# Optimization experiments

Hardware: AMD Instinct MI355X
Metric: run time of the kernel (lower is better)

## Reference

```python
import jax, jax.numpy as jnp
import numpy as np

N_EDGES = 1_000_000
N_PARTICLES = 50_000
NUM_RADIAL = 16
EMBED = 128
OUT_EMBED = 256
NUM_TARGETS = 1


def setup_inputs() -> dict:
    key = jax.random.key(0)
    ks = jax.random.split(key, 12)
    s = lambda fan_in: 1.0 / np.sqrt(fan_in)
    inp = {
        'messages': jax.random.normal(ks[0], (N_EDGES, EMBED), jnp.float32),
        'rbf': jax.random.normal(ks[1], (N_EDGES, NUM_RADIAL), jnp.float32),
        'idx_i': jax.random.randint(ks[2], (N_EDGES,), 0, N_PARTICLES),
        'idx_j': jax.random.randint(ks[3], (N_EDGES,), 0, N_PARTICLES),
        'W_rbf': jax.random.normal(ks[4], (NUM_RADIAL, EMBED), jnp.float32) * s(NUM_RADIAL),
        'W_up': jax.random.normal(ks[5], (EMBED, OUT_EMBED), jnp.float32) * s(EMBED),
        'W1': jax.random.normal(ks[6], (OUT_EMBED, OUT_EMBED), jnp.float32) * s(OUT_EMBED),
        'b1': jnp.zeros((OUT_EMBED,), jnp.float32),
        'W2': jax.random.normal(ks[7], (OUT_EMBED, OUT_EMBED), jnp.float32) * s(OUT_EMBED),
        'b2': jnp.zeros((OUT_EMBED,), jnp.float32),
        'W3': jax.random.normal(ks[8], (OUT_EMBED, OUT_EMBED), jnp.float32) * s(OUT_EMBED),
        'b3': jnp.zeros((OUT_EMBED,), jnp.float32),
        'W_final': jax.random.normal(ks[9], (OUT_EMBED, NUM_TARGETS), jnp.float32) * s(OUT_EMBED),
    }
    return inp


def reference(messages, rbf, idx_i, idx_j, W_rbf, W_up, W1, b1, W2, b2, W3, b3, W_final):
    # RBF gate: [E, NUM_RADIAL] @ [NUM_RADIAL, EMBED] -> [E, EMBED]
    transformed_rbf = rbf @ W_rbf
    gated = messages * transformed_rbf  # elementwise, [E, EMBED]
    # scatter-add per receiving atom idx_i -> [N_PARTICLES, EMBED]
    summed = jax.ops.segment_sum(gated, idx_i, num_segments=N_PARTICLES)
    h = summed @ W_up
    h = jax.nn.swish(h @ W1 + b1)
    h = jax.nn.swish(h @ W2 + b2)
    h = jax.nn.swish(h @ W3 + b3)
    per_atom_targets = h @ W_final  # [N_PARTICLES, NUM_TARGETS]
    return per_atom_targets
```

## Files before the change

kernel.cpp:

```cpp
#include <hip/hip_runtime.h>
#include <hip/hip_bf16.h>

#define EMBED 128
#define NRAD  16
#define OUTE  256

typedef __bf16 bf16x8 __attribute__((ext_vector_type(8)));
typedef float  f32x4  __attribute__((ext_vector_type(4)));

static __device__ __forceinline__ unsigned short f2bf(float x) {
    return __builtin_bit_cast(unsigned short, (__bf16)x);
}

__global__ __launch_bounds__(256) void zero_fill_kernel(uint4* __restrict__ dst, int n4)
{
    const uint4 z = {0u, 0u, 0u, 0u};
    for (int i = blockIdx.x * blockDim.x + threadIdx.x; i < n4;
         i += gridDim.x * blockDim.x)
        dst[i] = z;
}

__global__ __launch_bounds__(256) void hist_kernel(const int* __restrict__ idx_i,
                                                   int* __restrict__ counts, int n_edges)
{
    for (int e = blockIdx.x * blockDim.x + threadIdx.x; e < n_edges;
         e += gridDim.x * blockDim.x)
        atomicAdd(&counts[idx_i[e]], 1);
}

__global__ __launch_bounds__(1024) void scan_kernel(const int* __restrict__ counts,
                                                    int* __restrict__ cursor, int n)
{
    __shared__ int partial[1024];
    const int tid = threadIdx.x;
    const int chunk = (n + 1023) / 1024;
    const int lo = min(tid * chunk, n), hi = min(lo + chunk, n);
    int s = 0;
    for (int i = lo; i < hi; ++i) s += counts[i];
    partial[tid] = s;
    __syncthreads();
    for (int off = 1; off < 1024; off <<= 1) {
        int v = (tid >= off) ? partial[tid - off] : 0;
        __syncthreads();
        partial[tid] += v;
        __syncthreads();
    }
    int run = (tid > 0) ? partial[tid - 1] : 0;
    for (int i = lo; i < hi; ++i) {
        cursor[i] = run;
        run += counts[i];
    }
}

__global__ __launch_bounds__(256) void scatter_ids_kernel(const int* __restrict__ idx_i,
                                                          int* __restrict__ cursor,
                                                          int* __restrict__ edge_order,
                                                          int* __restrict__ pid_sorted,
                                                          int n_edges)
{
    for (int e = blockIdx.x * blockDim.x + threadIdx.x; e < n_edges;
         e += gridDim.x * blockDim.x) {
        const int i = idx_i[e];
        const int pos = atomicAdd(&cursor[i], 1);
        edge_order[pos] = e;
        pid_sorted[pos] = i;
    }
}

__device__ __forceinline__ float2 rbf_dot(float4 q0, float4 q1, float4 q2, float4 q3,
                                          const float2* w)
{
    const float rv[NRAD] = {q0.x, q0.y, q0.z, q0.w, q1.x, q1.y, q1.z, q1.w,
                            q2.x, q2.y, q2.z, q2.w, q3.x, q3.y, q3.z, q3.w};
    float tx = 0.f, ty = 0.f;
#pragma unroll
    for (int r = 0; r < NRAD; ++r) {
        tx = fmaf(rv[r], w[r].x, tx);
        ty = fmaf(rv[r], w[r].y, ty);
    }
    return make_float2(tx, ty);
}

#define SEGSTEP(P, M, T)                                                    \
    do {                                                                    \
        if ((P) != cur) {                                                   \
            if (first) {                                                    \
                atomicAdd(&summed[(long long)cur * EMBED + col], ax);       \
                atomicAdd(&summed[(long long)cur * EMBED + col + 1], ay);   \
                first = false;                                              \
            } else {                                                        \
                *reinterpret_cast<float2*>(                                 \
                    &summed[(long long)cur * EMBED + col]) =                \
                    make_float2(ax, ay);                                    \
            }                                                               \
            ax = 0.f; ay = 0.f; cur = (P);                                  \
        }                                                                   \
        ax = fmaf((M).x, (T).x, ax);                                        \
        ay = fmaf((M).y, (T).y, ay);                                        \
    } while (0)

__global__ __launch_bounds__(256, 4) void gated_segsum_kernel(
    const float* __restrict__ messages, const float* __restrict__ rbf,
    const int* __restrict__ edge_order, const int* __restrict__ pid_sorted,
    const float* __restrict__ W_rbf, float* __restrict__ summed, int n_edges)
{
    const int lane = threadIdx.x & 63;
    const int wv   = threadIdx.x >> 6;
    const int col  = lane * 2;

    float2 w[NRAD];
#pragma unroll
    for (int r = 0; r < NRAD; ++r)
        w[r] = *reinterpret_cast<const float2*>(&W_rbf[r * EMBED + col]);

    const int nwin = (n_edges + 63) >> 6;
    for (int win = blockIdx.x * 4 + wv; win < nwin; win += gridDim.x * 4) {
        const int w0 = win << 6;
        const int nq = min(n_edges - w0, 64);

        float ax = 0.f, ay = 0.f;
        int  cur   = pid_sorted[w0];
        bool first = true;

        int q = 0;
        for (; q + 4 <= nq; q += 4) {
            const int b = w0 + q;
            const int e0 = edge_order[b + 0];
            const int e1 = edge_order[b + 1];
            const int e2 = edge_order[b + 2];
            const int e3 = edge_order[b + 3];
            const int p0 = pid_sorted[b + 0];
            const int p1 = pid_sorted[b + 1];
            const int p2 = pid_sorted[b + 2];
            const int p3 = pid_sorted[b + 3];

            const float2 m0 = *reinterpret_cast<const float2*>(
                messages + (long long)e0 * EMBED + col);
            const float2 m1 = *reinterpret_cast<const float2*>(
                messages + (long long)e1 * EMBED + col);
            const float2 m2 = *reinterpret_cast<const float2*>(
                messages + (long long)e2 * EMBED + col);
            const float2 m3 = *reinterpret_cast<const float2*>(
                messages + (long long)e3 * EMBED + col);

            const float4* R0 = reinterpret_cast<const float4*>(rbf + (long long)e0 * NRAD);
            const float4* R1 = reinterpret_cast<const float4*>(rbf + (long long)e1 * NRAD);
            const float4* R2 = reinterpret_cast<const float4*>(rbf + (long long)e2 * NRAD);
            const float4* R3 = reinterpret_cast<const float4*>(rbf + (long long)e3 * NRAD);
            const float2 t0 = rbf_dot(R0[0], R0[1], R0[2], R0[3], w);
            const float2 t1 = rbf_dot(R1[0], R1[1], R1[2], R1[3], w);
            const float2 t2 = rbf_dot(R2[0], R2[1], R2[2], R2[3], w);
            const float2 t3 = rbf_dot(R3[0], R3[1], R3[2], R3[3], w);

            SEGSTEP(p0, m0, t0);
            SEGSTEP(p1, m1, t1);
            SEGSTEP(p2, m2, t2);
            SEGSTEP(p3, m3, t3);
        }
        for (; q < nq; ++q) {
            const int b = w0 + q;
            const int e = edge_order[b];
            const int p = pid_sorted[b];
            const float2 m = *reinterpret_cast<const float2*>(
                messages + (long long)e * EMBED + col);
            const float4* R = reinterpret_cast<const float4*>(rbf + (long long)e * NRAD);
            const float2 t = rbf_dot(R[0], R[1], R[2], R[3], w);
            SEGSTEP(p, m, t);
        }

        atomicAdd(&summed[(long long)cur * EMBED + col], ax);
        atomicAdd(&summed[(long long)cur * EMBED + col + 1], ay);
    }
}

__global__ __launch_bounds__(256) void prep_weights_kernel(
    const float* __restrict__ Wup, const float* __restrict__ W1,
    const float* __restrict__ W2, const float* __restrict__ W3,
    __bf16* __restrict__ WupT, __bf16* __restrict__ W1T,
    __bf16* __restrict__ W2T, __bf16* __restrict__ W3T)
{
    const int total = OUTE * EMBED + 3 * OUTE * OUTE;
    for (int id = blockIdx.x * blockDim.x + threadIdx.x; id < total;
         id += gridDim.x * blockDim.x) {
        if (id < OUTE * EMBED) {
            const int n = id / EMBED, k = id % EMBED;
            WupT[id] = (__bf16)Wup[k * OUTE + n];
        } else {
            const int r = id - OUTE * EMBED;
            const int wsel = r / (OUTE * OUTE);
            const int rr = r % (OUTE * OUTE);
            const int n = rr / OUTE, k = rr % OUTE;
            const float* src = (wsel == 0) ? W1 : ((wsel == 1) ? W2 : W3);
            __bf16* dst = (wsel == 0) ? W1T : ((wsel == 1) ? W2T : W3T);
            dst[rr] = (__bf16)src[k * OUTE + n];
        }
    }
}

template <int K, bool ACT>
__device__ __forceinline__ void mlp_layer(const unsigned short* lin, unsigned short* lout,
                                          const __bf16* __restrict__ Wt,
                                          const float* __restrict__ bias, int l, int w)
{
    f32x4 acc[4][4];
#pragma unroll
    for (int i = 0; i < 4; ++i)
#pragma unroll
        for (int j = 0; j < 4; ++j)
            acc[i][j] = (f32x4){0.f, 0.f, 0.f, 0.f};

    const int lr = l & 15;
    const int hi = l >> 4;
    const int kg = hi * 8;

#pragma unroll
    for (int kk = 0; kk < K; kk += 32) {
        bf16x8 af[4], bf_[4];
#pragma unroll
        for (int i = 0; i < 4; ++i) {
            const int row = i * 16 + lr;
            const int byte = row * 512 + (((kk + kg) * 2) ^ ((row & 7) << 4));
            af[i] = *reinterpret_cast<const bf16x8*>(
                reinterpret_cast<const char*>(lin) + byte);
        }
#pragma unroll
        for (int j = 0; j < 4; ++j) {
            const int n = w * 64 + j * 16 + lr;
            bf_[j] = *reinterpret_cast<const bf16x8*>(Wt + (size_t)n * K + kk + kg);
        }
#pragma unroll
        for (int i = 0; i < 4; ++i)
#pragma unroll
            for (int j = 0; j < 4; ++j)
                acc[i][j] = __builtin_amdgcn_mfma_f32_16x16x32_bf16(af[i], bf_[j],
                                                                    acc[i][j], 0, 0, 0);
    }

    float bb[4];
#pragma unroll
    for (int j = 0; j < 4; ++j)
        bb[j] = ACT ? bias[w * 64 + j * 16 + lr] : 0.f;

#pragma unroll
    for (int j = 0; j < 4; ++j) {
        const int colb = (w * 64 + j * 16 + lr) * 2;
#pragma unroll
        for (int i = 0; i < 4; ++i) {
#pragma unroll
            for (int r = 0; r < 4; ++r) {
                const int row = i * 16 + hi * 4 + r;
                float v = acc[i][j][r];
                if (ACT) {
                    v += bb[j];
                    v = v / (1.f + __expf(-v));
                }
                const int byte = row * 512 + (colb ^ ((row & 7) << 4));
                *reinterpret_cast<unsigned short*>(
                    reinterpret_cast<char*>(lout) + byte) = f2bf(v);
            }
        }
    }
}

__global__ __launch_bounds__(256) void fused_mlp_kernel(
    const float* __restrict__ summed,
    const __bf16* __restrict__ WupT, const __bf16* __restrict__ W1T,
    const __bf16* __restrict__ W2T, const __bf16* __restrict__ W3T,
    const float* __restrict__ b1, const float* __restrict__ b2,
    const float* __restrict__ b3, const float* __restrict__ Wf,
    float* __restrict__ out, int M)
{
    __shared__ __align__(16) unsigned short buf0[64 * 256];
    __shared__ __align__(16) unsigned short buf1[64 * 256];

    const int tid = threadIdx.x;
    const int l = tid & 63, w = tid >> 6;
    const int row0 = blockIdx.x * 64;

#pragma unroll
    for (int i = 0; i < 8; ++i) {
        const int id = tid + i * 256;
        const int row = id >> 5;
        const int c = (id & 31) * 4;
        float4 v = make_float4(0.f, 0.f, 0.f, 0.f);
        const int gr = row0 + row;
        if (gr < M)
            v = *reinterpret_cast<const float4*>(summed + (long long)gr * EMBED + c);
        ushort4 u = make_ushort4(f2bf(v.x), f2bf(v.y), f2bf(v.z), f2bf(v.w));
        const int byte = row * 512 + ((c * 2) ^ ((row & 7) << 4));
        *reinterpret_cast<ushort4*>(reinterpret_cast<char*>(buf0) + byte) = u;
    }
    __syncthreads();

    mlp_layer<EMBED, false>(buf0, buf1, WupT, nullptr, l, w);
    __syncthreads();
    mlp_layer<OUTE, true>(buf1, buf0, W1T, b1, l, w);
    __syncthreads();
    mlp_layer<OUTE, true>(buf0, buf1, W2T, b2, l, w);
    __syncthreads();
    mlp_layer<OUTE, true>(buf1, buf0, W3T, b3, l, w);
    __syncthreads();

    const int row = tid >> 2, q = tid & 3;
    float s = 0.f;
#pragma unroll
    for (int c = 0; c < 8; ++c) {
        const int k = q * 64 + c * 8;
        const int byte = row * 512 + ((k * 2) ^ ((row & 7) << 4));
        const bf16x8 hv = *reinterpret_cast<const bf16x8*>(
            reinterpret_cast<const char*>(buf0) + byte);
        const float4 wa = *reinterpret_cast<const float4*>(Wf + k);
        const float4 wb = *reinterpret_cast<const float4*>(Wf + k + 4);
        s += (float)hv[0] * wa.x + (float)hv[1] * wa.y +
             (float)hv[2] * wa.z + (float)hv[3] * wa.w +
             (float)hv[4] * wb.x + (float)hv[5] * wb.y +
             (float)hv[6] * wb.z + (float)hv[7] * wb.w;
    }
    s += __shfl_xor(s, 1);
    s += __shfl_xor(s, 2);
    if (q == 0 && row0 + row < M) out[row0 + row] = s;
}

extern "C" void kernel_launch(void* const* d_in, const int* in_sizes, int n_in,
                              void* d_out, int out_size, void* d_ws, size_t ws_size,
                              hipStream_t stream)
{
    const float* messages = (const float*)d_in[0];
    const float* rbf      = (const float*)d_in[1];
    const int*   idx_i    = (const int*)d_in[2];
    const float* W_rbf    = (const float*)d_in[4];
    const float* W_up     = (const float*)d_in[5];
    const float* W1       = (const float*)d_in[6];
    const float* b1       = (const float*)d_in[7];
    const float* W2       = (const float*)d_in[8];
    const float* b2       = (const float*)d_in[9];
    const float* W3       = (const float*)d_in[10];
    const float* b3       = (const float*)d_in[11];
    const float* Wf       = (const float*)d_in[12];
    float* out = (float*)d_out;

    const int n_edges = in_sizes[2];
    const int M = out_size;

    char* ws = (char*)d_ws;
    size_t off = 0;
    float* summed = (float*)(ws + off); off += (size_t)M * EMBED * sizeof(float);
    int* counts     = (int*)(ws + off); off += (size_t)M * sizeof(int);
    int* cursor     = (int*)(ws + off); off += (size_t)M * sizeof(int);
    int* edge_order = (int*)(ws + off); off += (size_t)n_edges * sizeof(int);
    int* pid_sorted = (int*)(ws + off); off += (size_t)n_edges * sizeof(int);
    off = (off + 255) & ~(size_t)255;
    __bf16* WupT = (__bf16*)(ws + off); off += (size_t)OUTE * EMBED * 2;
    __bf16* W1T  = (__bf16*)(ws + off); off += (size_t)OUTE * OUTE * 2;
    __bf16* W2T  = (__bf16*)(ws + off); off += (size_t)OUTE * OUTE * 2;
    __bf16* W3T  = (__bf16*)(ws + off); off += (size_t)OUTE * OUTE * 2;

    const int n4 = (int)(((size_t)M * EMBED + M) / 4);
    zero_fill_kernel<<<2048, 256, 0, stream>>>((uint4*)summed, n4);

    hist_kernel<<<4096, 256, 0, stream>>>(idx_i, counts, n_edges);
    scan_kernel<<<1, 1024, 0, stream>>>(counts, cursor, M);
    scatter_ids_kernel<<<4096, 256, 0, stream>>>(idx_i, cursor, edge_order,
                                                 pid_sorted, n_edges);
    prep_weights_kernel<<<896, 256, 0, stream>>>(W_up, W1, W2, W3, WupT, W1T, W2T, W3T);
    gated_segsum_kernel<<<2048, 256, 0, stream>>>(messages, rbf, edge_order, pid_sorted,
                                                  W_rbf, summed, n_edges);
    fused_mlp_kernel<<<(M + 63) / 64, 256, 0, stream>>>(summed, WupT, W1T, W2T, W3T,
                                                        b1, b2, b3, Wf, out, M);
}
```

Measured before the change: 536.1 us.

## Software-pipeline gated segsum with shuffled indices and next-group prefetch

For full 64-edge windows, each lane now loads one edge index and particle id, and these are broadcast with wave shuffles instead of repeated scalar loads. The message and rbf gathers for the next group of four edges are issued before the current group is accumulated, so gather latency overlaps with the segment reduction. Launch bounds occupancy drops from 4 to 3 blocks per CU to leave room for the extra prefetch registers, which may reduce latency hiding across waves.

```diff
diff --git a/kernel.cpp b/kernel.cpp
--- a/kernel.cpp
+++ b/kernel.cpp
@@ -99,7 +99,22 @@
         ay = fmaf((M).y, (T).y, ay);                                        \
     } while (0)
 
-__global__ __launch_bounds__(256, 4) void gated_segsum_kernel(
+#define PREF_IDS(J)                                                         \
+    eN##J = __shfl(myE, qn + J, 64);                                        \
+    pN##J = __shfl(myP, qn + J, 64);
+
+#define PREF_LOAD(J)                                                        \
+    mN##J = *reinterpret_cast<const float2*>(                               \
+        messages + (long long)eN##J * EMBED + col);                         \
+    {                                                                       \
+        const float4* R_ =                                                  \
+            reinterpret_cast<const float4*>(rbf + (long long)eN##J * NRAD); \
+        rA##J = R_[0]; rB##J = R_[1]; rC##J = R_[2]; rD##J = R_[3];         \
+    }
+
+#define PREF_DOT(J) tN##J = rbf_dot(rA##J, rB##J, rC##J, rD##J, w);
+
+__global__ __launch_bounds__(256, 3) void gated_segsum_kernel(
     const float* __restrict__ messages, const float* __restrict__ rbf,
     const int* __restrict__ edge_order, const int* __restrict__ pid_sorted,
     const float* __restrict__ W_rbf, float* __restrict__ summed, int n_edges)
@@ -119,57 +134,64 @@
         const int nq = min(n_edges - w0, 64);
 
         float ax = 0.f, ay = 0.f;
-        int  cur   = pid_sorted[w0];
         bool first = true;
 
-        int q = 0;
-        for (; q + 4 <= nq; q += 4) {
-            const int b = w0 + q;
-            const int e0 = edge_order[b + 0];
-            const int e1 = edge_order[b + 1];
-            const int e2 = edge_order[b + 2];
-            const int e3 = edge_order[b + 3];
-            const int p0 = pid_sorted[b + 0];
-            const int p1 = pid_sorted[b + 1];
-            const int p2 = pid_sorted[b + 2];
-            const int p3 = pid_sorted[b + 3];
-
-            const float2 m0 = *reinterpret_cast<const float2*>(
-                messages + (long long)e0 * EMBED + col);
-            const float2 m1 = *reinterpret_cast<const float2*>(
-                messages + (long long)e1 * EMBED + col);
-            const float2 m2 = *reinterpret_cast<const float2*>(
-                messages + (long long)e2 * EMBED + col);
-            const float2 m3 = *reinterpret_cast<const float2*>(
-                messages + (long long)e3 * EMBED + col);
-
-            const float4* R0 = reinterpret_cast<const float4*>(rbf + (long long)e0 * NRAD);
-            const float4* R1 = reinterpret_cast<const float4*>(rbf + (long long)e1 * NRAD);
-            const float4* R2 = reinterpret_cast<const float4*>(rbf + (long long)e2 * NRAD);
-            const float4* R3 = reinterpret_cast<const float4*>(rbf + (long long)e3 * NRAD);
-            const float2 t0 = rbf_dot(R0[0], R0[1], R0[2], R0[3], w);
-            const float2 t1 = rbf_dot(R1[0], R1[1], R1[2], R1[3], w);
-            const float2 t2 = rbf_dot(R2[0], R2[1], R2[2], R2[3], w);
-            const float2 t3 = rbf_dot(R3[0], R3[1], R3[2], R3[3], w);
-
-            SEGSTEP(p0, m0, t0);
-            SEGSTEP(p1, m1, t1);
-            SEGSTEP(p2, m2, t2);
-            SEGSTEP(p3, m3, t3);
-        }
-        for (; q < nq; ++q) {
-            const int b = w0 + q;
-            const int e = edge_order[b];
-            const int p = pid_sorted[b];
-            const float2 m = *reinterpret_cast<const float2*>(
-                messages + (long long)e * EMBED + col);
-            const float4* R = reinterpret_cast<const float4*>(rbf + (long long)e * NRAD);
-            const float2 t = rbf_dot(R[0], R[1], R[2], R[3], w);
-            SEGSTEP(p, m, t);
-        }
-
-        atomicAdd(&summed[(long long)cur * EMBED + col], ax);
-        atomicAdd(&summed[(long long)cur * EMBED + col + 1], ay);
+        if (nq == 64) {
+            const int myE = edge_order[w0 + lane];
+            const int myP = pid_sorted[w0 + lane];
+            int cur = __shfl(myP, 0, 64);
+
+            int eN0, eN1, eN2, eN3, pN0, pN1, pN2, pN3;
+            float2 mN0, mN1, mN2, mN3, tN0, tN1, tN2, tN3;
+            float4 rA0, rB0, rC0, rD0, rA1, rB1, rC1, rD1;
+            float4 rA2, rB2, rC2, rD2, rA3, rB3, rC3, rD3;
+            float2 m0, m1, m2, m3, t0, t1, t2, t3;
+            int p0, p1, p2, p3;
+
+            int qn = 0;
+            PREF_IDS(0) PREF_IDS(1) PREF_IDS(2) PREF_IDS(3)
+            PREF_LOAD(0) PREF_LOAD(1) PREF_LOAD(2) PREF_LOAD(3)
+            PREF_DOT(0) PREF_DOT(1) PREF_DOT(2) PREF_DOT(3)
+            m0 = mN0; m1 = mN1; m2 = mN2; m3 = mN3;
+            t0 = tN0; t1 = tN1; t2 = tN2; t3 = tN3;
+            p0 = pN0; p1 = pN1; p2 = pN2; p3 = pN3;
+
+            for (int q = 0; q < 64; q += 4) {
+                const bool more = (q + 4) < 64;
+                if (more) {
+                    qn = q + 4;
+                    PREF_IDS(0) PREF_IDS(1) PREF_IDS(2) PREF_IDS(3)
+                    PREF_LOAD(0) PREF_LOAD(1) PREF_LOAD(2) PREF_LOAD(3)
+                }
+                SEGSTEP(p0, m0, t0);
+                SEGSTEP(p1, m1, t1);
+                SEGSTEP(p2, m2, t2);
+                SEGSTEP(p3, m3, t3);
+                if (more) {
+                    PREF_DOT(0) PREF_DOT(1) PREF_DOT(2) PREF_DOT(3)
+                    m0 = mN0; m1 = mN1; m2 = mN2; m3 = mN3;
+                    t0 = tN0; t1 = tN1; t2 = tN2; t3 = tN3;
+                    p0 = pN0; p1 = pN1; p2 = pN2; p3 = pN3;
+                }
+            }
+            atomicAdd(&summed[(long long)cur * EMBED + col], ax);
+            atomicAdd(&summed[(long long)cur * EMBED + col + 1], ay);
+        } else {
+            int cur = pid_sorted[w0];
+            for (int q = 0; q < nq; ++q) {
+                const int b = w0 + q;
+                const int e = edge_order[b];
+                const int p = pid_sorted[b];
+                const float2 m = *reinterpret_cast<const float2*>(
+                    messages + (long long)e * EMBED + col);
+                const float4* R =
+                    reinterpret_cast<const float4*>(rbf + (long long)e * NRAD);
+                const float2 t = rbf_dot(R[0], R[1], R[2], R[3], w);
+                SEGSTEP(p, m, t);
+            }
+            atomicAdd(&summed[(long long)cur * EMBED + col], ax);
+            atomicAdd(&summed[(long long)cur * EMBED + col + 1], ay);
+        }
     }
 }
 
```

Result: faster. 515.0 us, median of 4 (-3.9%).

## Pack edge/particle ids, load rbf once per lane and prefetch message rows

Applied to the files above, without the earlier changes.

Edge ids and particle ids are interleaved into one int2 array, so each 64-edge window takes a single coalesced load. Each lane then loads one edge's rbf row, and the values are broadcast with readlane. Before, every lane redundantly loaded all 16 rbf floats for every edge. Message rows are software-pipelined two groups ahead using shuffled edge ids, to hide gather latency, at the cost of more registers and many readlane/shuffle instructions.

```diff
diff --git a/kernel.cpp b/kernel.cpp
--- a/kernel.cpp
+++ b/kernel.cpp
@@ -11,6 +11,9 @@
 static __device__ __forceinline__ unsigned short f2bf(float x) {
     return __builtin_bit_cast(unsigned short, (__bf16)x);
 }
+
+#define RLF(X, L) __builtin_bit_cast(float, \
+    __builtin_amdgcn_readlane(__builtin_bit_cast(int, (X)), (L)))
 
 __global__ __launch_bounds__(256) void zero_fill_kernel(uint4* __restrict__ dst, int n4)
 {
@@ -54,31 +57,15 @@
 
 __global__ __launch_bounds__(256) void scatter_ids_kernel(const int* __restrict__ idx_i,
                                                           int* __restrict__ cursor,
-                                                          int* __restrict__ edge_order,
-                                                          int* __restrict__ pid_sorted,
+                                                          int2* __restrict__ eid_pid,
                                                           int n_edges)
 {
     for (int e = blockIdx.x * blockDim.x + threadIdx.x; e < n_edges;
          e += gridDim.x * blockDim.x) {
         const int i = idx_i[e];
         const int pos = atomicAdd(&cursor[i], 1);
-        edge_order[pos] = e;
-        pid_sorted[pos] = i;
-    }
-}
-
-__device__ __forceinline__ float2 rbf_dot(float4 q0, float4 q1, float4 q2, float4 q3,
-                                          const float2* w)
-{
-    const float rv[NRAD] = {q0.x, q0.y, q0.z, q0.w, q1.x, q1.y, q1.z, q1.w,
-                            q2.x, q2.y, q2.z, q2.w, q3.x, q3.y, q3.z, q3.w};
-    float tx = 0.f, ty = 0.f;
-#pragma unroll
-    for (int r = 0; r < NRAD; ++r) {
-        tx = fmaf(rv[r], w[r].x, tx);
-        ty = fmaf(rv[r], w[r].y, ty);
-    }
-    return make_float2(tx, ty);
+        eid_pid[pos] = make_int2(e, i);
+    }
 }
 
 #define SEGSTEP(P, M, T)                                                    \
@@ -99,9 +86,47 @@
         ay = fmaf((M).y, (T).y, ay);                                        \
     } while (0)
 
+#define MSG_ISSUE(S, QPOS)                                                  \
+    {                                                                       \
+        const int eT0 = __shfl(myE, (QPOS) + 0, 64);                        \
+        const int eT1 = __shfl(myE, (QPOS) + 1, 64);                        \
+        const int eT2 = __shfl(myE, (QPOS) + 2, 64);                        \
+        const int eT3 = __shfl(myE, (QPOS) + 3, 64);                        \
+        S##0 = *reinterpret_cast<const float2*>(                            \
+            messages + (long long)eT0 * EMBED + col);                       \
+        S##1 = *reinterpret_cast<const float2*>(                            \
+            messages + (long long)eT1 * EMBED + col);                       \
+        S##2 = *reinterpret_cast<const float2*>(                            \
+            messages + (long long)eT2 * EMBED + col);                       \
+        S##3 = *reinterpret_cast<const float2*>(                            \
+            messages + (long long)eT3 * EMBED + col);                       \
+    }
+
+#define DOT_EDGE(TX, TY, L)                                                      \
+    {                                                                            \
+        float v_;                                                                \
+        TX = 0.f; TY = 0.f;                                                      \
+        v_ = RLF(ra.x, L); TX = fmaf(v_, w[0].x, TX);  TY = fmaf(v_, w[0].y, TY);  \
+        v_ = RLF(ra.y, L); TX = fmaf(v_, w[1].x, TX);  TY = fmaf(v_, w[1].y, TY);  \
+        v_ = RLF(ra.z, L); TX = fmaf(v_, w[2].x, TX);  TY = fmaf(v_, w[2].y, TY);  \
+        v_ = RLF(ra.w, L); TX = fmaf(v_, w[3].x, TX);  TY = fmaf(v_, w[3].y, TY);  \
+        v_ = RLF(rb.x, L); TX = fmaf(v_, w[4].x, TX);  TY = fmaf(v_, w[4].y, TY);  \
+        v_ = RLF(rb.y, L); TX = fmaf(v_, w[5].x, TX);  TY = fmaf(v_, w[5].y, TY);  \
+        v_ = RLF(rb.z, L); TX = fmaf(v_, w[6].x, TX);  TY = fmaf(v_, w[6].y, TY);  \
+        v_ = RLF(rb.w, L); TX = fmaf(v_, w[7].x, TX);  TY = fmaf(v_, w[7].y, TY);  \
+        v_ = RLF(rc.x, L); TX = fmaf(v_, w[8].x, TX);  TY = fmaf(v_, w[8].y, TY);  \
+        v_ = RLF(rc.y, L); TX = fmaf(v_, w[9].x, TX);  TY = fmaf(v_, w[9].y, TY);  \
+        v_ = RLF(rc.z, L); TX = fmaf(v_, w[10].x, TX); TY = fmaf(v_, w[10].y, TY); \
+        v_ = RLF(rc.w, L); TX = fmaf(v_, w[11].x, TX); TY = fmaf(v_, w[11].y, TY); \
+        v_ = RLF(rd.x, L); TX = fmaf(v_, w[12].x, TX); TY = fmaf(v_, w[12].y, TY); \
+        v_ = RLF(rd.y, L); TX = fmaf(v_, w[13].x, TX); TY = fmaf(v_, w[13].y, TY); \
+        v_ = RLF(rd.z, L); TX = fmaf(v_, w[14].x, TX); TY = fmaf(v_, w[14].y, TY); \
+        v_ = RLF(rd.w, L); TX = fmaf(v_, w[15].x, TX); TY = fmaf(v_, w[15].y, TY); \
+    }
+
 __global__ __launch_bounds__(256, 4) void gated_segsum_kernel(
     const float* __restrict__ messages, const float* __restrict__ rbf,
-    const int* __restrict__ edge_order, const int* __restrict__ pid_sorted,
+    const int2* __restrict__ eid_pid,
     const float* __restrict__ W_rbf, float* __restrict__ summed, int n_edges)
 {
     const int lane = threadIdx.x & 63;
@@ -119,57 +144,72 @@
         const int nq = min(n_edges - w0, 64);
 
         float ax = 0.f, ay = 0.f;
-        int  cur   = pid_sorted[w0];
         bool first = true;
 
-        int q = 0;
-        for (; q + 4 <= nq; q += 4) {
-            const int b = w0 + q;
-            const int e0 = edge_order[b + 0];
-            const int e1 = edge_order[b + 1];
-            const int e2 = edge_order[b + 2];
-            const int e3 = edge_order[b + 3];
-            const int p0 = pid_sorted[b + 0];
-            const int p1 = pid_sorted[b + 1];
-            const int p2 = pid_sorted[b + 2];
-            const int p3 = pid_sorted[b + 3];
-
-            const float2 m0 = *reinterpret_cast<const float2*>(
-                messages + (long long)e0 * EMBED + col);
-            const float2 m1 = *reinterpret_cast<const float2*>(
-                messages + (long long)e1 * EMBED + col);
-            const float2 m2 = *reinterpret_cast<const float2*>(
-                messages + (long long)e2 * EMBED + col);
-            const float2 m3 = *reinterpret_cast<const float2*>(
-                messages + (long long)e3 * EMBED + col);
-
-            const float4* R0 = reinterpret_cast<const float4*>(rbf + (long long)e0 * NRAD);
-            const float4* R1 = reinterpret_cast<const float4*>(rbf + (long long)e1 * NRAD);
-            const float4* R2 = reinterpret_cast<const float4*>(rbf + (long long)e2 * NRAD);
-            const float4* R3 = reinterpret_cast<const float4*>(rbf + (long long)e3 * NRAD);
-            const float2 t0 = rbf_dot(R0[0], R0[1], R0[2], R0[3], w);
-            const float2 t1 = rbf_dot(R1[0], R1[1], R1[2], R1[3], w);
-            const float2 t2 = rbf_dot(R2[0], R2[1], R2[2], R2[3], w);
-            const float2 t3 = rbf_dot(R3[0], R3[1], R3[2], R3[3], w);
-
-            SEGSTEP(p0, m0, t0);
-            SEGSTEP(p1, m1, t1);
-            SEGSTEP(p2, m2, t2);
-            SEGSTEP(p3, m3, t3);
+        if (nq == 64) {
+            const int2 ep = eid_pid[w0 + lane];
+            const int myE = ep.x;
+            const int myP = ep.y;
+            int cur = __builtin_amdgcn_readlane(myP, 0);
+
+            const float4* R = reinterpret_cast<const float4*>(rbf + (long long)myE * NRAD);
+            const float4 ra = R[0], rb = R[1], rc = R[2], rd = R[3];
+
+            float2 cA0, cA1, cA2, cA3, cB0, cB1, cB2, cB3, cC0, cC1, cC2, cC3;
+            MSG_ISSUE(cA, 0)
+            MSG_ISSUE(cB, 4)
+
+            for (int q = 0; q < 16; ++q) {
+                if (q < 14) { MSG_ISSUE(cC, (q + 2) * 4) }
+
+                const int base = q * 4;
+                float t0x, t0y, t1x, t1y, t2x, t2y, t3x, t3y;
+                DOT_EDGE(t0x, t0y, base + 0)
+                DOT_EDGE(t1x, t1y, base + 1)
+                DOT_EDGE(t2x, t2y, base + 2)
+                DOT_EDGE(t3x, t3y, base + 3)
+                const int p0 = __builtin_amdgcn_readlane(myP, base + 0);
+                const int p1 = __builtin_amdgcn_readlane(myP, base + 1);
+                const int p2 = __builtin_amdgcn_readlane(myP, base + 2);
+                const int p3 = __builtin_amdgcn_readlane(myP, base + 3);
+                const float2 t0 = make_float2(t0x, t0y);
+                const float2 t1 = make_float2(t1x, t1y);
+                const float2 t2 = make_float2(t2x, t2y);
+                const float2 t3 = make_float2(t3x, t3y);
+
+                SEGSTEP(p0, cA0, t0);
+                SEGSTEP(p1, cA1, t1);
+                SEGSTEP(p2, cA2, t2);
+                SEGSTEP(p3, cA3, t3);
+
+                cA0 = cB0; cA1 = cB1; cA2 = cB2; cA3 = cB3;
+                cB0 = cC0; cB1 = cC1; cB2 = cC2; cB3 = cC3;
+            }
+            atomicAdd(&summed[(long long)cur * EMBED + col], ax);
+            atomicAdd(&summed[(long long)cur * EMBED + col + 1], ay);
+        } else {
+            int cur = eid_pid[w0].y;
+            for (int q = 0; q < nq; ++q) {
+                const int2 ep = eid_pid[w0 + q];
+                const float2 m = *reinterpret_cast<const float2*>(
+                    messages + (long long)ep.x * EMBED + col);
+                const float4* R =
+                    reinterpret_cast<const float4*>(rbf + (long long)ep.x * NRAD);
+                const float4 q0 = R[0], q1 = R[1], q2 = R[2], q3 = R[3];
+                const float rv[NRAD] = {q0.x, q0.y, q0.z, q0.w, q1.x, q1.y, q1.z, q1.w,
+                                        q2.x, q2.y, q2.z, q2.w, q3.x, q3.y, q3.z, q3.w};
+                float tx = 0.f, ty = 0.f;
+#pragma unroll
+                for (int r = 0; r < NRAD; ++r) {
+                    tx = fmaf(rv[r], w[r].x, tx);
+                    ty = fmaf(rv[r], w[r].y, ty);
+                }
+                const float2 t = make_float2(tx, ty);
+                SEGSTEP(ep.y, m, t);
+            }
+            atomicAdd(&summed[(long long)cur * EMBED + col], ax);
+            atomicAdd(&summed[(long long)cur * EMBED + col + 1], ay);
         }
-        for (; q < nq; ++q) {
-            const int b = w0 + q;
-            const int e = edge_order[b];
-            const int p = pid_sorted[b];
-            const float2 m = *reinterpret_cast<const float2*>(
-                messages + (long long)e * EMBED + col);
-            const float4* R = reinterpret_cast<const float4*>(rbf + (long long)e * NRAD);
-            const float2 t = rbf_dot(R[0], R[1], R[2], R[3], w);
-            SEGSTEP(p, m, t);
-        }
-
-        atomicAdd(&summed[(long long)cur * EMBED + col], ax);
-        atomicAdd(&summed[(long long)cur * EMBED + col + 1], ay);
     }
 }
 
@@ -347,8 +387,8 @@
     float* summed = (float*)(ws + off); off += (size_t)M * EMBED * sizeof(float);
     int* counts     = (int*)(ws + off); off += (size_t)M * sizeof(int);
     int* cursor     = (int*)(ws + off); off += (size_t)M * sizeof(int);
-    int* edge_order = (int*)(ws + off); off += (size_t)n_edges * sizeof(int);
-    int* pid_sorted = (int*)(ws + off); off += (size_t)n_edges * sizeof(int);
+    off = (off + 7) & ~(size_t)7;
+    int2* eid_pid   = (int2*)(ws + off); off += (size_t)n_edges * sizeof(int2);
     off = (off + 255) & ~(size_t)255;
     __bf16* WupT = (__bf16*)(ws + off); off += (size_t)OUTE * EMBED * 2;
     __bf16* W1T  = (__bf16*)(ws + off); off += (size_t)OUTE * OUTE * 2;
@@ -360,10 +400,9 @@
 
     hist_kernel<<<4096, 256, 0, stream>>>(idx_i, counts, n_edges);
     scan_kernel<<<1, 1024, 0, stream>>>(counts, cursor, M);
-    scatter_ids_kernel<<<4096, 256, 0, stream>>>(idx_i, cursor, edge_order,
-                                                 pid_sorted, n_edges);
+    scatter_ids_kernel<<<4096, 256, 0, stream>>>(idx_i, cursor, eid_pid, n_edges);
     prep_weights_kernel<<<896, 256, 0, stream>>>(W_up, W1, W2, W3, WupT, W1T, W2T, W3T);
-    gated_segsum_kernel<<<2048, 256, 0, stream>>>(messages, rbf, edge_order, pid_sorted,
+    gated_segsum_kernel<<<2048, 256, 0, stream>>>(messages, rbf, eid_pid,
                                                   W_rbf, summed, n_edges);
     fused_mlp_kernel<<<(M + 63) / 64, 256, 0, stream>>>(summed, WupT, W1T, W2T, W3T,
                                                         b1, b2, b3, Wf, out, M);
```

After: 454.9 us. 15.2% less time.
